# Optimization experiments

Hardware: AMD Instinct MI355X
Metric: run time of the kernel (lower is better)

Reference implementation:

```python
import jax, jax.numpy as jnp
import numpy as np

NEG_SLOPE = 0.2  # PyG GATConv default negative_slope
BN_EPS = 1e-5


def gat_layer(x, src, dst, W, b, a_src, a_dst, heads, out_ch, concat):
    # x: [N, Fin]; W: [Fin, heads*out_ch]; a_src/a_dst: [heads, out_ch]
    N = x.shape[0]
    h = (x @ W).reshape(N, heads, out_ch)
    s = (h * a_src).sum(-1)            # [N, H]
    d = (h * a_dst).sum(-1)            # [N, H]
    e = jax.nn.leaky_relu(s[src] + d[dst], NEG_SLOPE)   # [E, H]
    # segment softmax over incoming edges of each destination node
    m = jax.ops.segment_max(e, dst, num_segments=N)
    ex = jnp.exp(e - m[dst])
    denom = jax.ops.segment_sum(ex, dst, num_segments=N)
    alpha = ex / (denom[dst] + 1e-16)                   # [E, H]
    out = jax.ops.segment_sum(alpha[:, :, None] * h[src], dst, num_segments=N)  # [N,H,C]
    out = out.reshape(N, heads * out_ch) if concat else out.mean(axis=1)
    return out + b


def batchnorm(x, gamma, beta):
    mu = x.mean(axis=0)
    var = x.var(axis=0)
    return gamma * (x - mu) * jax.lax.rsqrt(var + BN_EPS) + beta


def setup_inputs() -> dict:
    key = jax.random.key(0)
    ks = jax.random.split(key, 24)
    N, E, Fin, Hd, heads, C = 50000, 800000, 128, 64, 4, 2
    wdim = Hd * heads  # 256
    inp = {
        'x': jax.random.normal(ks[0], (N, Fin), jnp.float32),
        'edge_index': jax.random.randint(ks[1], (2, E), 0, N, jnp.int64),
    }
    def glorot(k, shape):
        fan = shape[0] + shape[-1]
        return jax.random.normal(k, shape, jnp.float32) * np.sqrt(2.0 / fan)
    # layer 0: Fin -> heads x Hd (concat)
    inp['W0'] = glorot(ks[2], (Fin, wdim)); inp['b0'] = jnp.zeros((wdim,), jnp.float32)
    inp['asrc0'] = glorot(ks[3], (heads, Hd)); inp['adst0'] = glorot(ks[4], (heads, Hd))
    inp['g0'] = jnp.ones((wdim,), jnp.float32); inp['be0'] = jnp.zeros((wdim,), jnp.float32)
    # layer 1: wdim -> heads x Hd (concat)
    inp['W1'] = glorot(ks[5], (wdim, wdim)); inp['b1'] = jnp.zeros((wdim,), jnp.float32)
    inp['asrc1'] = glorot(ks[6], (heads, Hd)); inp['adst1'] = glorot(ks[7], (heads, Hd))
    inp['g1'] = jnp.ones((wdim,), jnp.float32); inp['be1'] = jnp.zeros((wdim,), jnp.float32)
    # layer 2: wdim -> 1 head x Hd (no concat)
    inp['W2'] = glorot(ks[8], (wdim, Hd)); inp['b2'] = jnp.zeros((Hd,), jnp.float32)
    inp['asrc2'] = glorot(ks[9], (1, Hd)); inp['adst2'] = glorot(ks[10], (1, Hd))
    inp['g2'] = jnp.ones((Hd,), jnp.float32); inp['be2'] = jnp.zeros((Hd,), jnp.float32)
    # classifier: Linear(2*Hd, Hd) -> ReLU -> Linear(Hd, C)
    inp['Wc1'] = glorot(ks[11], (2 * Hd, Hd)); inp['bc1'] = jnp.zeros((Hd,), jnp.float32)
    inp['Wc2'] = glorot(ks[12], (Hd, C)); inp['bc2'] = jnp.zeros((C,), jnp.float32)
    return inp


def reference(x, edge_index, W0, b0, asrc0, adst0, g0, be0,
              W1, b1, asrc1, adst1, g1, be1,
              W2, b2, asrc2, adst2, g2, be2,
              Wc1, bc1, Wc2, bc2):
    N = x.shape[0]
    # add self-loops (PyG GATConv default)
    loops = jnp.arange(N, dtype=edge_index.dtype)
    src = jnp.concatenate([edge_index[0], loops])
    dst = jnp.concatenate([edge_index[1], loops])
    heads, Hd = asrc0.shape[0], asrc0.shape[1]

    h = gat_layer(x, src, dst, W0, b0, asrc0, adst0, heads, Hd, True)
    h = jax.nn.relu(batchnorm(h, g0, be0))
    h = gat_layer(h, src, dst, W1, b1, asrc1, adst1, heads, Hd, True)
    h = jax.nn.relu(batchnorm(h, g1, be1))
    h = gat_layer(h, src, dst, W2, b2, asrc2, adst2, 1, Hd, False)
    h = jax.nn.relu(batchnorm(h, g2, be2))

    pooled = jnp.concatenate([h.mean(axis=0, keepdims=True),
                              h.max(axis=0, keepdims=True)], axis=1)  # [1, 2*Hd]
    z = jax.nn.relu(pooled @ Wc1 + bc1)
    return z @ Wc2 + bc2  # [1, num_classes]
```

## Files before the change

### kernel.cpp

```cpp
#include <hip/hip_runtime.h>


typedef unsigned int uint;
typedef unsigned short ushort;

#define NEG_SLOPE 0.2f
#define BN_EPS 1e-5f
#define NB_RED 64

__device__ __forceinline__ float bf2f(uint u) { return __uint_as_float(u << 16); }
__device__ __forceinline__ ushort f2bf(float f) {
    uint u = __float_as_uint(f);
    u += 0x7fff + ((u >> 16) & 1);
    return (ushort)(u >> 16);
}
__device__ __forceinline__ float lrelu(float x) { return x > 0.f ? x : NEG_SLOPE * x; }


__global__ void prep_kernel(const float* __restrict__ x, ushort* __restrict__ xb,
                            int total_real, int total_pad,
                            const float* __restrict__ W0, ushort* __restrict__ w0t,
                            const float* __restrict__ W1, ushort* __restrict__ w1t,
                            const float* __restrict__ W2, ushort* __restrict__ w2t,
                            const int* __restrict__ ei, int* __restrict__ deg, int E) {
    int i = blockIdx.x * blockDim.x + threadIdx.x;
    if (i < total_pad) {
        xb[i] = (i < total_real) ? f2bf(x[i]) : (ushort)0;
        return;
    }
    int j = i - total_pad;
    if (j < 32768) {
        int n = j / 128, k = j - n * 128;
        w0t[j] = f2bf(W0[(size_t)k * 256 + n]);
        return;
    }
    j -= 32768;
    if (j < 65536) {
        int n = j / 256, k = j - n * 256;
        w1t[j] = f2bf(W1[(size_t)k * 256 + n]);
        return;
    }
    j -= 65536;
    if (j < 16384) {
        int n = j / 256, k = j - n * 256;
        w2t[j] = f2bf(W2[(size_t)k * 64 + n]);
        return;
    }
    j -= 16384;
    if (j < E) atomicAdd(&deg[ei[E + j]], 1);
}


__global__ void scan_part(const int* __restrict__ deg, int* __restrict__ offsets,
                          int* __restrict__ bsum, int N) {
    __shared__ int sh[256];
    int t = threadIdx.x;
    int base = blockIdx.x * 1024 + t * 4;
    int v0 = (base + 0 < N) ? deg[base + 0] : 0;
    int v1 = (base + 1 < N) ? deg[base + 1] : 0;
    int v2 = (base + 2 < N) ? deg[base + 2] : 0;
    int v3 = (base + 3 < N) ? deg[base + 3] : 0;
    int s = v0 + v1 + v2 + v3;
    sh[t] = s;
    __syncthreads();
    for (int off = 1; off < 256; off <<= 1) {
        int y = (t >= off) ? sh[t - off] : 0;
        __syncthreads();
        sh[t] += y;
        __syncthreads();
    }
    int p = sh[t] - s;
    if (base + 0 < N) offsets[base + 0] = p;
    p += v0;
    if (base + 1 < N) offsets[base + 1] = p;
    p += v1;
    if (base + 2 < N) offsets[base + 2] = p;
    p += v2;
    if (base + 3 < N) offsets[base + 3] = p;
    if (t == 255) bsum[blockIdx.x] = sh[255];
}

__global__ void scan_add(int* __restrict__ offsets, int* __restrict__ cursor,
                         const int* __restrict__ bsum, int N) {
    __shared__ int sadd;
    int nb = gridDim.x;
    if (threadIdx.x == 0) {
        int run = 0;
        for (int b = 0; b < (int)blockIdx.x; ++b) run += bsum[b];
        sadd = run;
        if ((int)blockIdx.x == nb - 1) {
            int tot = run;
            for (int b = blockIdx.x; b < nb; ++b) tot += bsum[b];
            offsets[N] = tot;
        }
    }
    __syncthreads();
    int add = sadd;
    int base = blockIdx.x * 1024 + threadIdx.x * 4;
#pragma unroll
    for (int k = 0; k < 4; ++k) {
        int i = base + k;
        if (i < N) { int v = offsets[i] + add; offsets[i] = v; cursor[i] = v; }
    }
}

__global__ void scatter_kernel(const int* __restrict__ ei, int* __restrict__ cursor,
                               int* __restrict__ srcs, int E) {
    int e = blockIdx.x * blockDim.x + threadIdx.x;
    if (e < E) {
        int s = ei[e];
        int d = ei[E + e];
        int p = atomicAdd(&cursor[d], 1);
        srcs[p] = s;
    }
}


typedef __attribute__((ext_vector_type(8))) short bf16x8;
typedef __attribute__((ext_vector_type(4))) float floatx4;

template <int BN, int H>
__launch_bounds__(256)
__global__ void mfma_gemm_bt(const ushort* __restrict__ A, const ushort* __restrict__ Bt,
                             ushort* __restrict__ C, const float* __restrict__ asrc,
                             const float* __restrict__ adst, float* __restrict__ sv,
                             float* __restrict__ dv, int K, int Nn) {
    constexpr int WCOLS = (BN == 128) ? 2 : 1;
    constexpr int WROWS = 4 / WCOLS;
    constexpr int MT = 128 / (WROWS * 16);
    constexpr int NT = BN / (WCOLS * 16);
    constexpr int BCALLS = (BN * 32 * 2) / 4096;

    __shared__ ushort As[128 * 32];
    __shared__ ushort Bs[BN * 32];

    int t = threadIdx.x;
    int w = t >> 6, l = t & 63;
    int row0 = blockIdx.x * 128;
    int col0 = blockIdx.y * BN;
    int wr = (w / WCOLS) * (MT * 16);
    int wc = (w % WCOLS) * (NT * 16);

    floatx4 acc[MT][NT];
#pragma unroll
    for (int mi = 0; mi < MT; ++mi)
#pragma unroll
        for (int ni = 0; ni < NT; ++ni)
#pragma unroll
            for (int r = 0; r < 4; ++r) acc[mi][ni][r] = 0.f;

    int mrow = l & 15;
    int kc = (l >> 4) * 8;

    for (int kt = 0; kt < K; kt += 32) {
#pragma unroll
        for (int c = 0; c < 2; ++c) {
            int idx = c * 256 + t;
            const ushort* gp = A + (size_t)(row0 + (idx >> 2)) * K + kt + (idx & 3) * 8;
            __builtin_amdgcn_global_load_lds(
                (const __attribute__((address_space(1))) void*)gp,
                (__attribute__((address_space(3))) void*)(As + (idx & ~63) * 8),
                16, 0, 0);
        }
#pragma unroll
        for (int c = 0; c < BCALLS; ++c) {
            int idx = c * 256 + t;
            const ushort* gp = Bt + (size_t)(col0 + (idx >> 2)) * K + kt + (idx & 3) * 8;
            __builtin_amdgcn_global_load_lds(
                (const __attribute__((address_space(1))) void*)gp,
                (__attribute__((address_space(3))) void*)(Bs + (idx & ~63) * 8),
                16, 0, 0);
        }
        __syncthreads();

        bf16x8 af[MT], bfr[NT];
#pragma unroll
        for (int mi = 0; mi < MT; ++mi)
            af[mi] = *(const bf16x8*)&As[(wr + mi * 16 + mrow) * 32 + kc];
#pragma unroll
        for (int ni = 0; ni < NT; ++ni)
            bfr[ni] = *(const bf16x8*)&Bs[(wc + ni * 16 + mrow) * 32 + kc];
#pragma unroll
        for (int mi = 0; mi < MT; ++mi)
#pragma unroll
            for (int ni = 0; ni < NT; ++ni)
                acc[mi][ni] = __builtin_amdgcn_mfma_f32_16x16x32_bf16(
                    af[mi], bfr[ni], acc[mi][ni], 0, 0, 0);
        __syncthreads();
    }

#pragma unroll
    for (int mi = 0; mi < MT; ++mi) {
        int rbase = row0 + wr + mi * 16 + (l >> 4) * 4;
#pragma unroll
        for (int ni = 0; ni < NT; ++ni) {
            int col = col0 + wc + ni * 16 + (l & 15);
#pragma unroll
            for (int r = 0; r < 4; ++r)
                C[(size_t)(rbase + r) * Nn + col] = f2bf(acc[mi][ni][r]);
        }
    }

    float av[NT], bv[NT];
#pragma unroll
    for (int ni = 0; ni < NT; ++ni) {
        int ch = col0 + wc + ni * 16 + (l & 15);
        av[ni] = asrc[ch];
        bv[ni] = adst[ch];
    }
    int gh = (col0 + wc) >> 6;
#pragma unroll
    for (int mi = 0; mi < MT; ++mi) {
#pragma unroll
        for (int r = 0; r < 4; ++r) {
            float s = 0.f, d = 0.f;
#pragma unroll
            for (int ni = 0; ni < NT; ++ni) {
                float hv = acc[mi][ni][r];
                s += hv * av[ni];
                d += hv * bv[ni];
            }
#pragma unroll
            for (int m = 8; m >= 1; m >>= 1) {
                s += __shfl_xor(s, m);
                d += __shfl_xor(d, m);
            }
            if ((l & 15) == 0) {
                int row = row0 + wr + mi * 16 + (l >> 4) * 4 + r;
                sv[row * H + gh] = s;
                dv[row * H + gh] = d;
            }
        }
    }
}


__launch_bounds__(128)
__global__ void agg4_kernel(const ushort* __restrict__ hb, const float* __restrict__ sv,
                            const float* __restrict__ dv, const int* __restrict__ offsets,
                            const int* __restrict__ srcs, const float* __restrict__ bias,
                            ushort* __restrict__ zb, int N) {
    __shared__ float lsum[4][32 * 9];
    __shared__ float lden[4][4];

    int i = blockIdx.x;
    int t = threadIdx.x;
    int grp = t >> 5, gl = t & 31;
    int head = gl >> 3;
    int beg = offsets[i], end = offsets[i + 1];

    float d_i = dv[i * 4 + head];
    float ax[8] = {};
    float den = 0.f;

    int j0 = beg + grp;
    int j1 = j0 + 4;
    while (j1 < end) {
        int s0 = srcs[j0], s1 = srcs[j1];
        float sv0 = sv[s0 * 4 + head];
        float sv1 = sv[s1 * 4 + head];
        uint4 q0 = *(const uint4*)&hb[(size_t)s0 * 256 + gl * 8];
        uint4 q1 = *(const uint4*)&hb[(size_t)s1 * 256 + gl * 8];
        float w0 = __expf(fminf(lrelu(sv0 + d_i), 60.f));
        float w1 = __expf(fminf(lrelu(sv1 + d_i), 60.f));
        den += w0 + w1;
        uint pr0[4] = {q0.x, q0.y, q0.z, q0.w};
        uint pr1[4] = {q1.x, q1.y, q1.z, q1.w};
#pragma unroll
        for (int k = 0; k < 4; ++k) {
            ax[2 * k]     += w0 * bf2f(pr0[k] & 0xffffu) + w1 * bf2f(pr1[k] & 0xffffu);
            ax[2 * k + 1] += w0 * bf2f(pr0[k] >> 16)     + w1 * bf2f(pr1[k] >> 16);
        }
        j0 += 8; j1 += 8;
    }
    if (j0 < end) {
        int s0 = srcs[j0];
        float sv0 = sv[s0 * 4 + head];
        uint4 q0 = *(const uint4*)&hb[(size_t)s0 * 256 + gl * 8];
        float w0 = __expf(fminf(lrelu(sv0 + d_i), 60.f));
        den += w0;
        uint pr0[4] = {q0.x, q0.y, q0.z, q0.w};
#pragma unroll
        for (int k = 0; k < 4; ++k) {
            ax[2 * k]     += w0 * bf2f(pr0[k] & 0xffffu);
            ax[2 * k + 1] += w0 * bf2f(pr0[k] >> 16);
        }
    }

#pragma unroll
    for (int k = 0; k < 8; ++k) lsum[grp][gl * 9 + k] = ax[k];
    if ((gl & 7) == 0) lden[grp][head] = den;
    __syncthreads();

    int h = t >> 5;
    int c0 = 2 * t, c1 = 2 * t + 1;
    int i0 = (c0 >> 3) * 9 + (c0 & 7);
    int i1 = (c1 >> 3) * 9 + (c1 & 7);
    float wself = __expf(fminf(lrelu(sv[i * 4 + h] + dv[i * 4 + h]), 60.f));
    float dtot = lden[0][h] + lden[1][h] + lden[2][h] + lden[3][h] + wself + 1e-16f;
    float rden = 1.f / dtot;
    uint p = *(const uint*)&hb[(size_t)i * 256 + c0];
    float a0 = lsum[0][i0] + lsum[1][i0] + lsum[2][i0] + lsum[3][i0]
             + wself * bf2f(p & 0xffffu);
    float a1 = lsum[0][i1] + lsum[1][i1] + lsum[2][i1] + lsum[3][i1]
             + wself * bf2f(p >> 16);
    a0 = a0 * rden + bias[c0];
    a1 = a1 * rden + bias[c1];
    *(uint*)&zb[(size_t)i * 256 + c0] = (uint)f2bf(a0) | ((uint)f2bf(a1) << 16);
}


__launch_bounds__(64)
__global__ void agg1_kernel(const ushort* __restrict__ hb, const float* __restrict__ sv,
                            const float* __restrict__ dv, const int* __restrict__ offsets,
                            const int* __restrict__ srcs, const float* __restrict__ bias,
                            ushort* __restrict__ zb, int N) {
    int i = blockIdx.x;
    int l = threadIdx.x;
    int grp = l >> 4, gl = l & 15;
    int beg = offsets[i], end = offsets[i + 1];

    float d_i = dv[i];
    float ax[4] = {};
    float den = 0.f;

    int j0 = beg + grp;
    int j1 = j0 + 4;
    while (j1 < end) {
        int s0 = srcs[j0], s1 = srcs[j1];
        float sv0 = sv[s0], sv1 = sv[s1];
        uint2 q0 = *(const uint2*)&hb[(size_t)s0 * 64 + gl * 4];
        uint2 q1 = *(const uint2*)&hb[(size_t)s1 * 64 + gl * 4];
        float w0 = __expf(fminf(lrelu(sv0 + d_i), 60.f));
        float w1 = __expf(fminf(lrelu(sv1 + d_i), 60.f));
        den += w0 + w1;
        ax[0] += w0 * bf2f(q0.x & 0xffffu) + w1 * bf2f(q1.x & 0xffffu);
        ax[1] += w0 * bf2f(q0.x >> 16)     + w1 * bf2f(q1.x >> 16);
        ax[2] += w0 * bf2f(q0.y & 0xffffu) + w1 * bf2f(q1.y & 0xffffu);
        ax[3] += w0 * bf2f(q0.y >> 16)     + w1 * bf2f(q1.y >> 16);
        j0 += 8; j1 += 8;
    }
    if (j0 < end) {
        int s0 = srcs[j0];
        float sv0 = sv[s0];
        uint2 q0 = *(const uint2*)&hb[(size_t)s0 * 64 + gl * 4];
        float w0 = __expf(fminf(lrelu(sv0 + d_i), 60.f));
        den += w0;
        ax[0] += w0 * bf2f(q0.x & 0xffffu);
        ax[1] += w0 * bf2f(q0.x >> 16);
        ax[2] += w0 * bf2f(q0.y & 0xffffu);
        ax[3] += w0 * bf2f(q0.y >> 16);
    }

#pragma unroll
    for (int k = 0; k < 4; ++k) {
        ax[k] += __shfl_xor(ax[k], 16);
        ax[k] += __shfl_xor(ax[k], 32);
    }
    den += __shfl_xor(den, 16);
    den += __shfl_xor(den, 32);

    if (l < 16) {
        float wself = __expf(fminf(lrelu(sv[i] + d_i), 60.f));
        float rden = 1.f / (den + wself + 1e-16f);
        uint2 q = *(const uint2*)&hb[(size_t)i * 64 + gl * 4];
        float a0 = (ax[0] + wself * bf2f(q.x & 0xffffu)) * rden + bias[gl * 4 + 0];
        float a1 = (ax[1] + wself * bf2f(q.x >> 16)) * rden + bias[gl * 4 + 1];
        float a2 = (ax[2] + wself * bf2f(q.y & 0xffffu)) * rden + bias[gl * 4 + 2];
        float a3 = (ax[3] + wself * bf2f(q.y >> 16)) * rden + bias[gl * 4 + 3];
        uint2 o;
        o.x = (uint)f2bf(a0) | ((uint)f2bf(a1) << 16);
        o.y = (uint)f2bf(a2) | ((uint)f2bf(a3) << 16);
        *(uint2*)&zb[(size_t)i * 64 + gl * 4] = o;
    }
}


template <int F>
__launch_bounds__(256)
__global__ void bn_stats_kernel(const ushort* __restrict__ x, float* __restrict__ ps,
                                float* __restrict__ pq, int N) {
    constexpr int OCT = F / 8;
    __shared__ float lds_s[F], lds_q[F];
    int t = threadIdx.x;
    if (t < F) { lds_s[t] = 0.f; lds_q[t] = 0.f; }
    __syncthreads();

    float s[8] = {}, q[8] = {};
    int total8 = N * F / 8;
    for (int idx = blockIdx.x * 256 + t; idx < total8; idx += NB_RED * 256) {
        uint4 v = ((const uint4*)x)[idx];
        uint pr[4] = {v.x, v.y, v.z, v.w};
#pragma unroll
        for (int k = 0; k < 4; ++k) {
            float a = bf2f(pr[k] & 0xffffu);
            float b = bf2f(pr[k] >> 16);
            s[2 * k] += a;     q[2 * k] += a * a;
            s[2 * k + 1] += b; q[2 * k + 1] += b * b;
        }
    }
    int co = t % OCT;
#pragma unroll
    for (int j = 0; j < 8; ++j) {
        atomicAdd(&lds_s[co * 8 + j], s[j]);
        atomicAdd(&lds_q[co * 8 + j], q[j]);
    }
    __syncthreads();
    if (t < F) {
        ps[blockIdx.x * F + t] = lds_s[t];
        pq[blockIdx.x * F + t] = lds_q[t];
    }
}

template <int F>
__launch_bounds__(256)
__global__ void bn_apply_kernel(uint* __restrict__ x, const float* __restrict__ ps,
                                const float* __restrict__ pq, const float* __restrict__ g,
                                const float* __restrict__ be, int N, int totalPairs) {
    __shared__ float ssc[F], ssh[F];
    int t = threadIdx.x;
    if (t < F) {
        float s = 0.f, q = 0.f;
        for (int b = 0; b < NB_RED; ++b) { s += ps[b * F + t]; q += pq[b * F + t]; }
        float mean = s / (float)N;
        float var = q / (float)N - mean * mean;
        float sc = g[t] * rsqrtf(var + BN_EPS);
        ssc[t] = sc;
        ssh[t] = be[t] - sc * mean;
    }
    __syncthreads();
    for (int i = blockIdx.x * 256 + t; i < totalPairs; i += gridDim.x * 256) {
        uint p = x[i];
        int c0 = (2 * i) & (F - 1);
        float v0 = fmaxf(bf2f(p & 0xffffu) * ssc[c0] + ssh[c0], 0.f);
        float v1 = fmaxf(bf2f(p >> 16) * ssc[c0 + 1] + ssh[c0 + 1], 0.f);
        x[i] = (uint)f2bf(v0) | ((uint)f2bf(v1) << 16);
    }
}


__launch_bounds__(256)
__global__ void pool_kernel(const ushort* __restrict__ y, const float* __restrict__ ps,
                            const float* __restrict__ pq, const float* __restrict__ g,
                            const float* __restrict__ be, float* __restrict__ psum,
                            float* __restrict__ pmax, int N) {
    constexpr int F = 64, OCT = 8;
    __shared__ float ssc[F], ssh[F];
    __shared__ float lds_s[F];
    __shared__ uint lds_m[F];
    int t = threadIdx.x;
    if (t < F) {
        float s = 0.f, q = 0.f;
        for (int b = 0; b < NB_RED; ++b) { s += ps[b * F + t]; q += pq[b * F + t]; }
        float mean = s / (float)N;
        float var = q / (float)N - mean * mean;
        float sc = g[t] * rsqrtf(var + BN_EPS);
        ssc[t] = sc;
        ssh[t] = be[t] - sc * mean;
        lds_s[t] = 0.f;
        lds_m[t] = 0u;
    }
    __syncthreads();

    int co = t % OCT;
    float sc[8], sh[8];
#pragma unroll
    for (int j = 0; j < 8; ++j) { sc[j] = ssc[co * 8 + j]; sh[j] = ssh[co * 8 + j]; }

    float s[8] = {}, m[8] = {};
    int total8 = N * F / 8;
    for (int idx = blockIdx.x * 256 + t; idx < total8; idx += NB_RED * 256) {
        uint4 v = ((const uint4*)y)[idx];
        uint pr[4] = {v.x, v.y, v.z, v.w};
#pragma unroll
        for (int k = 0; k < 4; ++k) {
            float a = fmaxf(bf2f(pr[k] & 0xffffu) * sc[2 * k] + sh[2 * k], 0.f);
            float b = fmaxf(bf2f(pr[k] >> 16) * sc[2 * k + 1] + sh[2 * k + 1], 0.f);
            s[2 * k] += a;     m[2 * k] = fmaxf(m[2 * k], a);
            s[2 * k + 1] += b; m[2 * k + 1] = fmaxf(m[2 * k + 1], b);
        }
    }
#pragma unroll
    for (int j = 0; j < 8; ++j) {
        atomicAdd(&lds_s[co * 8 + j], s[j]);
        atomicMax(&lds_m[co * 8 + j], __float_as_uint(m[j]));
    }
    __syncthreads();
    if (t < F) {
        psum[blockIdx.x * F + t] = lds_s[t];
        pmax[blockIdx.x * F + t] = __uint_as_float(lds_m[t]);
    }
}

__global__ void classify_kernel(const float* __restrict__ psum, const float* __restrict__ pmax,
                                const float* __restrict__ Wc1, const float* __restrict__ bc1,
                                const float* __restrict__ Wc2, const float* __restrict__ bc2,
                                float* __restrict__ out, int N) {
    __shared__ float pooled[128];
    __shared__ float z[64];
    int t = threadIdx.x;
    if (t < 64) {
        float s = 0.f;
        for (int b = 0; b < NB_RED; ++b) s += psum[b * 64 + t];
        pooled[t] = s / (float)N;
    } else {
        int c = t - 64;
        float m = 0.f;
        for (int b = 0; b < NB_RED; ++b) m = fmaxf(m, pmax[b * 64 + c]);
        pooled[t] = m;
    }
    __syncthreads();
    if (t < 64) {
        float a = bc1[t];
        for (int k = 0; k < 128; ++k) a += pooled[k] * Wc1[k * 64 + t];
        z[t] = a > 0.f ? a : 0.f;
    }
    __syncthreads();
    if (t < 2) {
        float a = bc2[t];
        for (int j = 0; j < 64; ++j) a += z[j] * Wc2[j * 2 + t];
        out[t] = a;
    }
}


extern "C" void kernel_launch(void* const* d_in, const int* in_sizes, int n_in,
                              void* d_out, int out_size, void* d_ws, size_t ws_size,
                              hipStream_t stream) {
    const float* x   = (const float*)d_in[0];
    const int*   ei  = (const int*)d_in[1];
    const float* W0  = (const float*)d_in[2];  const float* b0  = (const float*)d_in[3];
    const float* as0 = (const float*)d_in[4];  const float* ad0 = (const float*)d_in[5];
    const float* g0  = (const float*)d_in[6];  const float* be0 = (const float*)d_in[7];
    const float* W1  = (const float*)d_in[8];  const float* b1  = (const float*)d_in[9];
    const float* as1 = (const float*)d_in[10]; const float* ad1 = (const float*)d_in[11];
    const float* g1  = (const float*)d_in[12]; const float* be1 = (const float*)d_in[13];
    const float* W2  = (const float*)d_in[14]; const float* b2  = (const float*)d_in[15];
    const float* as2 = (const float*)d_in[16]; const float* ad2 = (const float*)d_in[17];
    const float* g2  = (const float*)d_in[18]; const float* be2 = (const float*)d_in[19];
    const float* Wc1 = (const float*)d_in[20]; const float* bc1 = (const float*)d_in[21];
    const float* Wc2 = (const float*)d_in[22]; const float* bc2 = (const float*)d_in[23];
    float* out = (float*)d_out;

    const int N = in_sizes[0] / 128;
    const int E = in_sizes[1] / 2;
    const int Mpad = ((N + 127) / 128) * 128;
    const int NB_SCAN = (N + 1023) / 1024;

    char* ws = (char*)d_ws;
    size_t o = 0;
    auto alloc = [&](size_t bytes) -> void* {
        void* p = ws + o;
        o = (o + bytes + 255) & ~(size_t)255;
        return p;
    };
    int*    deg     = (int*)alloc((size_t)N * 4);
    int*    offsets = (int*)alloc((size_t)(N + 1) * 4);
    int*    cursor  = (int*)alloc((size_t)N * 4);
    int*    srcs    = (int*)alloc((size_t)E * 4);
    int*    bsum    = (int*)alloc((size_t)NB_SCAN * 4);
    ushort* xb      = (ushort*)alloc((size_t)Mpad * 128 * 2);
    ushort* w0t     = (ushort*)alloc((size_t)256 * 128 * 2);
    ushort* w1t     = (ushort*)alloc((size_t)256 * 256 * 2);
    ushort* w2t     = (ushort*)alloc((size_t)64 * 256 * 2);
    ushort* hb      = (ushort*)alloc((size_t)Mpad * 256 * 2);
    ushort* zb      = (ushort*)alloc((size_t)Mpad * 256 * 2);
    float*  sv      = (float*)alloc((size_t)Mpad * 4 * 4);
    float*  dv      = (float*)alloc((size_t)Mpad * 4 * 4);
    float*  ps      = (float*)alloc((size_t)NB_RED * 256 * 4);
    float*  pq      = (float*)alloc((size_t)NB_RED * 256 * 4);
    float*  psum    = (float*)alloc((size_t)NB_RED * 64 * 4);
    float*  pmax    = (float*)alloc((size_t)NB_RED * 64 * 4);

    hipMemsetAsync(deg, 0, (size_t)N * 4, stream);
    int prep_total = Mpad * 128 + 32768 + 65536 + 16384 + E;
    prep_kernel<<<(prep_total + 255) / 256, 256, 0, stream>>>(
        x, xb, N * 128, Mpad * 128, W0, w0t, W1, w1t, W2, w2t, ei, deg, E);

    scan_part<<<NB_SCAN, 256, 0, stream>>>(deg, offsets, bsum, N);
    scan_add<<<NB_SCAN, 256, 0, stream>>>(offsets, cursor, bsum, N);
    scatter_kernel<<<(E + 255) / 256, 256, 0, stream>>>(ei, cursor, srcs, E);

    {
        dim3 gg(Mpad / 128, 2);
        mfma_gemm_bt<128, 4><<<gg, 256, 0, stream>>>(xb, w0t, hb, as0, ad0, sv, dv, 128, 256);
        agg4_kernel<<<N, 128, 0, stream>>>(hb, sv, dv, offsets, srcs, b0, zb, N);
        bn_stats_kernel<256><<<NB_RED, 256, 0, stream>>>(zb, ps, pq, N);
        bn_apply_kernel<256><<<256, 256, 0, stream>>>((uint*)zb, ps, pq, g0, be0, N, N * 128);
    }
    {
        dim3 gg(Mpad / 128, 2);
        mfma_gemm_bt<128, 4><<<gg, 256, 0, stream>>>(zb, w1t, hb, as1, ad1, sv, dv, 256, 256);
        agg4_kernel<<<N, 128, 0, stream>>>(hb, sv, dv, offsets, srcs, b1, zb, N);
        bn_stats_kernel<256><<<NB_RED, 256, 0, stream>>>(zb, ps, pq, N);
        bn_apply_kernel<256><<<256, 256, 0, stream>>>((uint*)zb, ps, pq, g1, be1, N, N * 128);
    }
    {
        dim3 gg(Mpad / 128, 1);
        mfma_gemm_bt<64, 1><<<gg, 256, 0, stream>>>(zb, w2t, hb, as2, ad2, sv, dv, 256, 64);
        agg1_kernel<<<N, 64, 0, stream>>>(hb, sv, dv, offsets, srcs, b2, zb, N);
        bn_stats_kernel<64><<<NB_RED, 256, 0, stream>>>(zb, ps, pq, N);
    }

    pool_kernel<<<NB_RED, 256, 0, stream>>>(zb, ps, pq, g2, be2, psum, pmax, N);
    classify_kernel<<<1, 128, 0, stream>>>(psum, pmax, Wc1, bc1, Wc2, bc2, out, N);
}
```

Baseline: 610.7 us.

## Fuse BatchNorm statistics into persistent wave-per-node aggregation kernels

The aggregation kernels become persistent grids of 1024 blocks, with one 64-lane wave per destination node and a grid-stride loop, instead of one block per node. Per-column sum and sum-of-squares for BatchNorm are accumulated in registers during aggregation and written as per-block partials, which removes the separate bn_stats pass over zb. A small bn_final kernel turns the partials into scale and shift, used by bn_apply and pool, and the pool grid is enlarged. This cuts one full read of the activations per layer and the per-node block launch and LDS reduction overhead. In exchange, each agg4 wave runs only two edges at a time per node, and the partial-sum reduction now runs over 1024 blocks.

```diff
diff --git a/kernel.cpp b/kernel.cpp
--- a/kernel.cpp
+++ b/kernel.cpp
@@ -6,7 +6,8 @@
 
 #define NEG_SLOPE 0.2f
 #define BN_EPS 1e-5f
-#define NB_RED 64
+#define NB_AGG 1024
+#define NB_POOL 256
 
 __device__ __forceinline__ float bf2f(uint u) { return __uint_as_float(u << 16); }
 __device__ __forceinline__ ushort f2bf(float f) {
@@ -235,199 +236,225 @@
 }
 
 
-__launch_bounds__(128)
+__launch_bounds__(256)
 __global__ void agg4_kernel(const ushort* __restrict__ hb, const float* __restrict__ sv,
                             const float* __restrict__ dv, const int* __restrict__ offsets,
                             const int* __restrict__ srcs, const float* __restrict__ bias,
-                            ushort* __restrict__ zb, int N) {
-    __shared__ float lsum[4][32 * 9];
-    __shared__ float lden[4][4];
-
-    int i = blockIdx.x;
-    int t = threadIdx.x;
-    int grp = t >> 5, gl = t & 31;
-    int head = gl >> 3;
-    int beg = offsets[i], end = offsets[i + 1];
-
-    float d_i = dv[i * 4 + head];
-    float ax[8] = {};
-    float den = 0.f;
-
-    int j0 = beg + grp;
-    int j1 = j0 + 4;
-    while (j1 < end) {
-        int s0 = srcs[j0], s1 = srcs[j1];
-        float sv0 = sv[s0 * 4 + head];
-        float sv1 = sv[s1 * 4 + head];
-        uint4 q0 = *(const uint4*)&hb[(size_t)s0 * 256 + gl * 8];
-        uint4 q1 = *(const uint4*)&hb[(size_t)s1 * 256 + gl * 8];
-        float w0 = __expf(fminf(lrelu(sv0 + d_i), 60.f));
-        float w1 = __expf(fminf(lrelu(sv1 + d_i), 60.f));
-        den += w0 + w1;
-        uint pr0[4] = {q0.x, q0.y, q0.z, q0.w};
-        uint pr1[4] = {q1.x, q1.y, q1.z, q1.w};
+                            ushort* __restrict__ zb, float* __restrict__ ps,
+                            float* __restrict__ pq, int N) {
+    __shared__ float lds_s[256], lds_q[256];
+    int t = threadIdx.x;
+    lds_s[t] = 0.f; lds_q[t] = 0.f;
+    __syncthreads();
+
+    int l = t & 63;
+    int half = l >> 5, gl = l & 31, head = gl >> 3;
+    int cbase = gl * 8;
+    int gw = blockIdx.x * 4 + (t >> 6);
+    int nw = gridDim.x * 4;
+
+    float bi[8];
+    *(float4*)&bi[0] = *(const float4*)&bias[cbase];
+    *(float4*)&bi[4] = *(const float4*)&bias[cbase + 4];
+
+    float szm[8] = {}, sqm[8] = {};
+
+    for (int i = gw; i < N; i += nw) {
+        int beg = offsets[i], end = offsets[i + 1];
+        float d_i = dv[i * 4 + head];
+        float acc[8] = {};
+        float den = 0.f;
+
+        int j0 = beg + half, j1 = j0 + 2;
+        while (j1 < end) {
+            int s0 = srcs[j0], s1 = srcs[j1];
+            float sv0 = sv[s0 * 4 + head], sv1 = sv[s1 * 4 + head];
+            uint4 q0 = *(const uint4*)&hb[(size_t)s0 * 256 + cbase];
+            uint4 q1 = *(const uint4*)&hb[(size_t)s1 * 256 + cbase];
+            float w0 = __expf(fminf(lrelu(sv0 + d_i), 60.f));
+            float w1 = __expf(fminf(lrelu(sv1 + d_i), 60.f));
+            den += w0 + w1;
+            uint pr0[4] = {q0.x, q0.y, q0.z, q0.w};
+            uint pr1[4] = {q1.x, q1.y, q1.z, q1.w};
+#pragma unroll
+            for (int k = 0; k < 4; ++k) {
+                acc[2 * k]     += w0 * bf2f(pr0[k] & 0xffffu) + w1 * bf2f(pr1[k] & 0xffffu);
+                acc[2 * k + 1] += w0 * bf2f(pr0[k] >> 16)     + w1 * bf2f(pr1[k] >> 16);
+            }
+            j0 += 4; j1 += 4;
+        }
+        if (j0 < end) {
+            int s0 = srcs[j0];
+            float sv0 = sv[s0 * 4 + head];
+            uint4 q0 = *(const uint4*)&hb[(size_t)s0 * 256 + cbase];
+            float w0 = __expf(fminf(lrelu(sv0 + d_i), 60.f));
+            den += w0;
+            uint pr0[4] = {q0.x, q0.y, q0.z, q0.w};
+#pragma unroll
+            for (int k = 0; k < 4; ++k) {
+                acc[2 * k]     += w0 * bf2f(pr0[k] & 0xffffu);
+                acc[2 * k + 1] += w0 * bf2f(pr0[k] >> 16);
+            }
+        }
+
+        den += __shfl_xor(den, 32);
+#pragma unroll
+        for (int k = 0; k < 8; ++k) acc[k] += __shfl_xor(acc[k], 32);
+
+        float wself = __expf(fminf(lrelu(sv[i * 4 + head] + d_i), 60.f));
+        uint4 qs = *(const uint4*)&hb[(size_t)i * 256 + cbase];
+        float rden = 1.f / (den + wself + 1e-16f);
+        uint prs[4] = {qs.x, qs.y, qs.z, qs.w};
+        float out[8];
 #pragma unroll
         for (int k = 0; k < 4; ++k) {
-            ax[2 * k]     += w0 * bf2f(pr0[k] & 0xffffu) + w1 * bf2f(pr1[k] & 0xffffu);
-            ax[2 * k + 1] += w0 * bf2f(pr0[k] >> 16)     + w1 * bf2f(pr1[k] >> 16);
-        }
-        j0 += 8; j1 += 8;
-    }
-    if (j0 < end) {
-        int s0 = srcs[j0];
-        float sv0 = sv[s0 * 4 + head];
-        uint4 q0 = *(const uint4*)&hb[(size_t)s0 * 256 + gl * 8];
-        float w0 = __expf(fminf(lrelu(sv0 + d_i), 60.f));
-        den += w0;
-        uint pr0[4] = {q0.x, q0.y, q0.z, q0.w};
-#pragma unroll
-        for (int k = 0; k < 4; ++k) {
-            ax[2 * k]     += w0 * bf2f(pr0[k] & 0xffffu);
-            ax[2 * k + 1] += w0 * bf2f(pr0[k] >> 16);
-        }
-    }
-
-#pragma unroll
-    for (int k = 0; k < 8; ++k) lsum[grp][gl * 9 + k] = ax[k];
-    if ((gl & 7) == 0) lden[grp][head] = den;
-    __syncthreads();
-
-    int h = t >> 5;
-    int c0 = 2 * t, c1 = 2 * t + 1;
-    int i0 = (c0 >> 3) * 9 + (c0 & 7);
-    int i1 = (c1 >> 3) * 9 + (c1 & 7);
-    float wself = __expf(fminf(lrelu(sv[i * 4 + h] + dv[i * 4 + h]), 60.f));
-    float dtot = lden[0][h] + lden[1][h] + lden[2][h] + lden[3][h] + wself + 1e-16f;
-    float rden = 1.f / dtot;
-    uint p = *(const uint*)&hb[(size_t)i * 256 + c0];
-    float a0 = lsum[0][i0] + lsum[1][i0] + lsum[2][i0] + lsum[3][i0]
-             + wself * bf2f(p & 0xffffu);
-    float a1 = lsum[0][i1] + lsum[1][i1] + lsum[2][i1] + lsum[3][i1]
-             + wself * bf2f(p >> 16);
-    a0 = a0 * rden + bias[c0];
-    a1 = a1 * rden + bias[c1];
-    *(uint*)&zb[(size_t)i * 256 + c0] = (uint)f2bf(a0) | ((uint)f2bf(a1) << 16);
-}
-
-
-__launch_bounds__(64)
+            out[2 * k]     = (acc[2 * k]     + wself * bf2f(prs[k] & 0xffffu)) * rden + bi[2 * k];
+            out[2 * k + 1] = (acc[2 * k + 1] + wself * bf2f(prs[k] >> 16))     * rden + bi[2 * k + 1];
+        }
+#pragma unroll
+        for (int k = 0; k < 8; ++k) { szm[k] += out[k]; sqm[k] += out[k] * out[k]; }
+        if (half == 0) {
+            uint4 o;
+            o.x = (uint)f2bf(out[0]) | ((uint)f2bf(out[1]) << 16);
+            o.y = (uint)f2bf(out[2]) | ((uint)f2bf(out[3]) << 16);
+            o.z = (uint)f2bf(out[4]) | ((uint)f2bf(out[5]) << 16);
+            o.w = (uint)f2bf(out[6]) | ((uint)f2bf(out[7]) << 16);
+            *(uint4*)&zb[(size_t)i * 256 + cbase] = o;
+        }
+    }
+
+    if (half == 0) {
+#pragma unroll
+        for (int k = 0; k < 8; ++k) {
+            atomicAdd(&lds_s[cbase + k], szm[k]);
+            atomicAdd(&lds_q[cbase + k], sqm[k]);
+        }
+    }
+    __syncthreads();
+    ps[blockIdx.x * 256 + t] = lds_s[t];
+    pq[blockIdx.x * 256 + t] = lds_q[t];
+}
+
+
+__launch_bounds__(256)
 __global__ void agg1_kernel(const ushort* __restrict__ hb, const float* __restrict__ sv,
                             const float* __restrict__ dv, const int* __restrict__ offsets,
                             const int* __restrict__ srcs, const float* __restrict__ bias,
-                            ushort* __restrict__ zb, int N) {
-    int i = blockIdx.x;
-    int l = threadIdx.x;
-    int grp = l >> 4, gl = l & 15;
-    int beg = offsets[i], end = offsets[i + 1];
-
-    float d_i = dv[i];
-    float ax[4] = {};
-    float den = 0.f;
-
-    int j0 = beg + grp;
-    int j1 = j0 + 4;
-    while (j1 < end) {
-        int s0 = srcs[j0], s1 = srcs[j1];
-        float sv0 = sv[s0], sv1 = sv[s1];
-        uint2 q0 = *(const uint2*)&hb[(size_t)s0 * 64 + gl * 4];
-        uint2 q1 = *(const uint2*)&hb[(size_t)s1 * 64 + gl * 4];
-        float w0 = __expf(fminf(lrelu(sv0 + d_i), 60.f));
-        float w1 = __expf(fminf(lrelu(sv1 + d_i), 60.f));
-        den += w0 + w1;
-        ax[0] += w0 * bf2f(q0.x & 0xffffu) + w1 * bf2f(q1.x & 0xffffu);
-        ax[1] += w0 * bf2f(q0.x >> 16)     + w1 * bf2f(q1.x >> 16);
-        ax[2] += w0 * bf2f(q0.y & 0xffffu) + w1 * bf2f(q1.y & 0xffffu);
-        ax[3] += w0 * bf2f(q0.y >> 16)     + w1 * bf2f(q1.y >> 16);
-        j0 += 8; j1 += 8;
-    }
-    if (j0 < end) {
-        int s0 = srcs[j0];
-        float sv0 = sv[s0];
-        uint2 q0 = *(const uint2*)&hb[(size_t)s0 * 64 + gl * 4];
-        float w0 = __expf(fminf(lrelu(sv0 + d_i), 60.f));
-        den += w0;
-        ax[0] += w0 * bf2f(q0.x & 0xffffu);
-        ax[1] += w0 * bf2f(q0.x >> 16);
-        ax[2] += w0 * bf2f(q0.y & 0xffffu);
-        ax[3] += w0 * bf2f(q0.y >> 16);
-    }
-
-#pragma unroll
-    for (int k = 0; k < 4; ++k) {
-        ax[k] += __shfl_xor(ax[k], 16);
-        ax[k] += __shfl_xor(ax[k], 32);
-    }
-    den += __shfl_xor(den, 16);
-    den += __shfl_xor(den, 32);
-
-    if (l < 16) {
+                            ushort* __restrict__ zb, float* __restrict__ ps,
+                            float* __restrict__ pq, int N) {
+    __shared__ float lds_s[64], lds_q[64];
+    int t = threadIdx.x;
+    if (t < 64) { lds_s[t] = 0.f; lds_q[t] = 0.f; }
+    __syncthreads();
+
+    int l = t & 63;
+    int slot = l >> 4, gl = l & 15;
+    int cbase = gl * 4;
+    int gw = blockIdx.x * 4 + (t >> 6);
+    int nw = gridDim.x * 4;
+
+    float bi[4];
+    *(float4*)&bi[0] = *(const float4*)&bias[cbase];
+
+    float szm[4] = {}, sqm[4] = {};
+
+    for (int i = gw; i < N; i += nw) {
+        int beg = offsets[i], end = offsets[i + 1];
+        float d_i = dv[i];
+        float acc[4] = {};
+        float den = 0.f;
+
+        int j0 = beg + slot, j1 = j0 + 4;
+        while (j1 < end) {
+            int s0 = srcs[j0], s1 = srcs[j1];
+            float sv0 = sv[s0], sv1 = sv[s1];
+            uint2 q0 = *(const uint2*)&hb[(size_t)s0 * 64 + cbase];
+            uint2 q1 = *(const uint2*)&hb[(size_t)s1 * 64 + cbase];
+            float w0 = __expf(fminf(lrelu(sv0 + d_i), 60.f));
+            float w1 = __expf(fminf(lrelu(sv1 + d_i), 60.f));
+            den += w0 + w1;
+            acc[0] += w0 * bf2f(q0.x & 0xffffu) + w1 * bf2f(q1.x & 0xffffu);
+            acc[1] += w0 * bf2f(q0.x >> 16)     + w1 * bf2f(q1.x >> 16);
+            acc[2] += w0 * bf2f(q0.y & 0xffffu) + w1 * bf2f(q1.y & 0xffffu);
+            acc[3] += w0 * bf2f(q0.y >> 16)     + w1 * bf2f(q1.y >> 16);
+            j0 += 8; j1 += 8;
+        }
+        if (j0 < end) {
+            int s0 = srcs[j0];
+            float sv0 = sv[s0];
+            uint2 q0 = *(const uint2*)&hb[(size_t)s0 * 64 + cbase];
+            float w0 = __expf(fminf(lrelu(sv0 + d_i), 60.f));
+            den += w0;
+            acc[0] += w0 * bf2f(q0.x & 0xffffu);
+            acc[1] += w0 * bf2f(q0.x >> 16);
+            acc[2] += w0 * bf2f(q0.y & 0xffffu);
+            acc[3] += w0 * bf2f(q0.y >> 16);
+        }
+
+#pragma unroll
+        for (int k = 0; k < 4; ++k) {
+            acc[k] += __shfl_xor(acc[k], 16);
+            acc[k] += __shfl_xor(acc[k], 32);
+        }
+        den += __shfl_xor(den, 16);
+        den += __shfl_xor(den, 32);
+
         float wself = __expf(fminf(lrelu(sv[i] + d_i), 60.f));
+        uint2 qs = *(const uint2*)&hb[(size_t)i * 64 + cbase];
         float rden = 1.f / (den + wself + 1e-16f);
-        uint2 q = *(const uint2*)&hb[(size_t)i * 64 + gl * 4];
-        float a0 = (ax[0] + wself * bf2f(q.x & 0xffffu)) * rden + bias[gl * 4 + 0];
-        float a1 = (ax[1] + wself * bf2f(q.x >> 16)) * rden + bias[gl * 4 + 1];
-        float a2 = (ax[2] + wself * bf2f(q.y & 0xffffu)) * rden + bias[gl * 4 + 2];
-        float a3 = (ax[3] + wself * bf2f(q.y >> 16)) * rden + bias[gl * 4 + 3];
-        uint2 o;
-        o.x = (uint)f2bf(a0) | ((uint)f2bf(a1) << 16);
-        o.y = (uint)f2bf(a2) | ((uint)f2bf(a3) << 16);
-        *(uint2*)&zb[(size_t)i * 64 + gl * 4] = o;
-    }
-}
-
-
-template <int F>
-__launch_bounds__(256)
-__global__ void bn_stats_kernel(const ushort* __restrict__ x, float* __restrict__ ps,
-                                float* __restrict__ pq, int N) {
-    constexpr int OCT = F / 8;
-    __shared__ float lds_s[F], lds_q[F];
-    int t = threadIdx.x;
-    if (t < F) { lds_s[t] = 0.f; lds_q[t] = 0.f; }
-    __syncthreads();
-
-    float s[8] = {}, q[8] = {};
-    int total8 = N * F / 8;
-    for (int idx = blockIdx.x * 256 + t; idx < total8; idx += NB_RED * 256) {
-        uint4 v = ((const uint4*)x)[idx];
-        uint pr[4] = {v.x, v.y, v.z, v.w};
+        float out[4];
+        out[0] = (acc[0] + wself * bf2f(qs.x & 0xffffu)) * rden + bi[0];
+        out[1] = (acc[1] + wself * bf2f(qs.x >> 16))     * rden + bi[1];
+        out[2] = (acc[2] + wself * bf2f(qs.y & 0xffffu)) * rden + bi[2];
+        out[3] = (acc[3] + wself * bf2f(qs.y >> 16))     * rden + bi[3];
+#pragma unroll
+        for (int k = 0; k < 4; ++k) { szm[k] += out[k]; sqm[k] += out[k] * out[k]; }
+        if (slot == 0) {
+            uint2 o;
+            o.x = (uint)f2bf(out[0]) | ((uint)f2bf(out[1]) << 16);
+            o.y = (uint)f2bf(out[2]) | ((uint)f2bf(out[3]) << 16);
+            *(uint2*)&zb[(size_t)i * 64 + cbase] = o;
+        }
+    }
+
+    if (slot == 0 && (l >> 4) == 0) {
 #pragma unroll
         for (int k = 0; k < 4; ++k) {
-            float a = bf2f(pr[k] & 0xffffu);
-            float b = bf2f(pr[k] >> 16);
-            s[2 * k] += a;     q[2 * k] += a * a;
-            s[2 * k + 1] += b; q[2 * k + 1] += b * b;
-        }
-    }
-    int co = t % OCT;
-#pragma unroll
-    for (int j = 0; j < 8; ++j) {
-        atomicAdd(&lds_s[co * 8 + j], s[j]);
-        atomicAdd(&lds_q[co * 8 + j], q[j]);
-    }
-    __syncthreads();
-    if (t < F) {
-        ps[blockIdx.x * F + t] = lds_s[t];
-        pq[blockIdx.x * F + t] = lds_q[t];
-    }
-}
-
-template <int F>
-__launch_bounds__(256)
-__global__ void bn_apply_kernel(uint* __restrict__ x, const float* __restrict__ ps,
-                                const float* __restrict__ pq, const float* __restrict__ g,
-                                const float* __restrict__ be, int N, int totalPairs) {
-    __shared__ float ssc[F], ssh[F];
+            atomicAdd(&lds_s[cbase + k], szm[k]);
+            atomicAdd(&lds_q[cbase + k], sqm[k]);
+        }
+    }
+    __syncthreads();
+    if (t < 64) {
+        ps[blockIdx.x * 64 + t] = lds_s[t];
+        pq[blockIdx.x * 64 + t] = lds_q[t];
+    }
+}
+
+
+__global__ void bn_final_kernel(const float* __restrict__ ps, const float* __restrict__ pq,
+                                const float* __restrict__ g, const float* __restrict__ be,
+                                float* __restrict__ scale, float* __restrict__ shift,
+                                int N, int F, int NB) {
     int t = threadIdx.x;
     if (t < F) {
         float s = 0.f, q = 0.f;
-        for (int b = 0; b < NB_RED; ++b) { s += ps[b * F + t]; q += pq[b * F + t]; }
+        for (int b = 0; b < NB; ++b) { s += ps[b * F + t]; q += pq[b * F + t]; }
         float mean = s / (float)N;
         float var = q / (float)N - mean * mean;
         float sc = g[t] * rsqrtf(var + BN_EPS);
-        ssc[t] = sc;
-        ssh[t] = be[t] - sc * mean;
-    }
+        scale[t] = sc;
+        shift[t] = be[t] - sc * mean;
+    }
+}
+
+template <int F>
+__launch_bounds__(256)
+__global__ void bn_apply_kernel(uint* __restrict__ x, const float* __restrict__ scale,
+                                const float* __restrict__ shift, int totalPairs) {
+    __shared__ float ssc[F], ssh[F];
+    int t = threadIdx.x;
+    if (t < F) { ssc[t] = scale[t]; ssh[t] = shift[t]; }
     __syncthreads();
     for (int i = blockIdx.x * 256 + t; i < totalPairs; i += gridDim.x * 256) {
         uint p = x[i];
@@ -440,36 +467,24 @@
 
 
 __launch_bounds__(256)
-__global__ void pool_kernel(const ushort* __restrict__ y, const float* __restrict__ ps,
-                            const float* __restrict__ pq, const float* __restrict__ g,
-                            const float* __restrict__ be, float* __restrict__ psum,
+__global__ void pool_kernel(const ushort* __restrict__ y, const float* __restrict__ scale,
+                            const float* __restrict__ shift, float* __restrict__ psum,
                             float* __restrict__ pmax, int N) {
     constexpr int F = 64, OCT = 8;
-    __shared__ float ssc[F], ssh[F];
     __shared__ float lds_s[F];
     __shared__ uint lds_m[F];
     int t = threadIdx.x;
-    if (t < F) {
-        float s = 0.f, q = 0.f;
-        for (int b = 0; b < NB_RED; ++b) { s += ps[b * F + t]; q += pq[b * F + t]; }
-        float mean = s / (float)N;
-        float var = q / (float)N - mean * mean;
-        float sc = g[t] * rsqrtf(var + BN_EPS);
-        ssc[t] = sc;
-        ssh[t] = be[t] - sc * mean;
-        lds_s[t] = 0.f;
-        lds_m[t] = 0u;
-    }
+    if (t < F) { lds_s[t] = 0.f; lds_m[t] = 0u; }
     __syncthreads();
 
     int co = t % OCT;
     float sc[8], sh[8];
 #pragma unroll
-    for (int j = 0; j < 8; ++j) { sc[j] = ssc[co * 8 + j]; sh[j] = ssh[co * 8 + j]; }
+    for (int j = 0; j < 8; ++j) { sc[j] = scale[co * 8 + j]; sh[j] = shift[co * 8 + j]; }
 
     float s[8] = {}, m[8] = {};
     int total8 = N * F / 8;
-    for (int idx = blockIdx.x * 256 + t; idx < total8; idx += NB_RED * 256) {
+    for (int idx = blockIdx.x * 256 + t; idx < total8; idx += NB_POOL * 256) {
         uint4 v = ((const uint4*)y)[idx];
         uint pr[4] = {v.x, v.y, v.z, v.w};
 #pragma unroll
@@ -501,12 +516,12 @@
     int t = threadIdx.x;
     if (t < 64) {
         float s = 0.f;
-        for (int b = 0; b < NB_RED; ++b) s += psum[b * 64 + t];
+        for (int b = 0; b < NB_POOL; ++b) s += psum[b * 64 + t];
         pooled[t] = s / (float)N;
     } else {
         int c = t - 64;
         float m = 0.f;
-        for (int b = 0; b < NB_RED; ++b) m = fmaxf(m, pmax[b * 64 + c]);
+        for (int b = 0; b < NB_POOL; ++b) m = fmaxf(m, pmax[b * 64 + c]);
         pooled[t] = m;
     }
     __syncthreads();
@@ -567,10 +582,12 @@
     ushort* zb      = (ushort*)alloc((size_t)Mpad * 256 * 2);
     float*  sv      = (float*)alloc((size_t)Mpad * 4 * 4);
     float*  dv      = (float*)alloc((size_t)Mpad * 4 * 4);
-    float*  ps      = (float*)alloc((size_t)NB_RED * 256 * 4);
-    float*  pq      = (float*)alloc((size_t)NB_RED * 256 * 4);
-    float*  psum    = (float*)alloc((size_t)NB_RED * 64 * 4);
-    float*  pmax    = (float*)alloc((size_t)NB_RED * 64 * 4);
+    float*  ps      = (float*)alloc((size_t)NB_AGG * 256 * 4);
+    float*  pq      = (float*)alloc((size_t)NB_AGG * 256 * 4);
+    float*  scale   = (float*)alloc(256 * 4);
+    float*  shift   = (float*)alloc(256 * 4);
+    float*  psum    = (float*)alloc((size_t)NB_POOL * 64 * 4);
+    float*  pmax    = (float*)alloc((size_t)NB_POOL * 64 * 4);
 
     hipMemsetAsync(deg, 0, (size_t)N * 4, stream);
     int prep_total = Mpad * 128 + 32768 + 65536 + 16384 + E;
@@ -584,24 +601,24 @@
     {
         dim3 gg(Mpad / 128, 2);
         mfma_gemm_bt<128, 4><<<gg, 256, 0, stream>>>(xb, w0t, hb, as0, ad0, sv, dv, 128, 256);
-        agg4_kernel<<<N, 128, 0, stream>>>(hb, sv, dv, offsets, srcs, b0, zb, N);
-        bn_stats_kernel<256><<<NB_RED, 256, 0, stream>>>(zb, ps, pq, N);
-        bn_apply_kernel<256><<<256, 256, 0, stream>>>((uint*)zb, ps, pq, g0, be0, N, N * 128);
+        agg4_kernel<<<NB_AGG, 256, 0, stream>>>(hb, sv, dv, offsets, srcs, b0, zb, ps, pq, N);
+        bn_final_kernel<<<1, 256, 0, stream>>>(ps, pq, g0, be0, scale, shift, N, 256, NB_AGG);
+        bn_apply_kernel<256><<<256, 256, 0, stream>>>((uint*)zb, scale, shift, N * 128);
     }
     {
         dim3 gg(Mpad / 128, 2);
         mfma_gemm_bt<128, 4><<<gg, 256, 0, stream>>>(zb, w1t, hb, as1, ad1, sv, dv, 256, 256);
-        agg4_kernel<<<N, 128, 0, stream>>>(hb, sv, dv, offsets, srcs, b1, zb, N);
-        bn_stats_kernel<256><<<NB_RED, 256, 0, stream>>>(zb, ps, pq, N);
-        bn_apply_kernel<256><<<256, 256, 0, stream>>>((uint*)zb, ps, pq, g1, be1, N, N * 128);
+        agg4_kernel<<<NB_AGG, 256, 0, stream>>>(hb, sv, dv, offsets, srcs, b1, zb, ps, pq, N);
+        bn_final_kernel<<<1, 256, 0, stream>>>(ps, pq, g1, be1, scale, shift, N, 256, NB_AGG);
+        bn_apply_kernel<256><<<256, 256, 0, stream>>>((uint*)zb, scale, shift, N * 128);
     }
     {
         dim3 gg(Mpad / 128, 1);
         mfma_gemm_bt<64, 1><<<gg, 256, 0, stream>>>(zb, w2t, hb, as2, ad2, sv, dv, 256, 64);
-        agg1_kernel<<<N, 64, 0, stream>>>(hb, sv, dv, offsets, srcs, b2, zb, N);
-        bn_stats_kernel<64><<<NB_RED, 256, 0, stream>>>(zb, ps, pq, N);
-    }
-
-    pool_kernel<<<NB_RED, 256, 0, stream>>>(zb, ps, pq, g2, be2, psum, pmax, N);
+        agg1_kernel<<<NB_AGG, 256, 0, stream>>>(hb, sv, dv, offsets, srcs, b2, zb, ps, pq, N);
+        bn_final_kernel<<<1, 64, 0, stream>>>(ps, pq, g2, be2, scale, shift, N, 64, NB_AGG);
+    }
+
+    pool_kernel<<<NB_POOL, 256, 0, stream>>>(zb, scale, shift, psum, pmax, N);
     classify_kernel<<<1, 128, 0, stream>>>(psum, pmax, Wc1, bc1, Wc2, bc2, out, N);
 }
```

New measurement: 1.377 ms. +125.5%, slower.
